# Optimization experiments

Measured on AMD Instinct MI355X. Metric: run time of the kernel, lower is better.

## Reference

```python
import jax, jax.numpy as jnp
import numpy as np

NODE_DIM = 128
OUT_DIM = 64
N_NODES = 50000
N_EDGES = 800000
NEG_SLOPE = 0.01  # F.leaky_relu default


def setup_inputs() -> dict:
    key = jax.random.key(0)
    k1, k2, k3, k4, k5 = jax.random.split(key, 5)
    h = jax.random.normal(k1, (N_NODES, NODE_DIM), dtype=jnp.float32)
    src = jax.random.randint(k2, (N_EDGES,), 0, N_NODES, dtype=jnp.int32)
    dst = jax.random.randint(k3, (N_EDGES,), 0, N_NODES, dtype=jnp.int32)
    # fc: Linear(node_dim, out_dim, bias=False); attn_fc: Linear(2*out_dim, 1, bias=False)
    W_fc = jax.random.normal(k4, (NODE_DIM, OUT_DIM), dtype=jnp.float32) * (1.0 / np.sqrt(NODE_DIM))
    W_attn = jax.random.normal(k5, (2 * OUT_DIM, 1), dtype=jnp.float32) * (1.0 / np.sqrt(2 * OUT_DIM))
    return {"h": h, "src": src, "dst": dst, "W_fc": W_fc, "W_attn": W_attn}


def reference(h, src, dst, W_fc, W_attn):
    N = h.shape[0]
    D = W_fc.shape[1]
    z = h @ W_fc                                   # [N, D]
    # attn_fc(concat(z_src, z_dst)) == z_src @ Wa[:D] + z_dst @ Wa[D:]
    s_src = (z @ W_attn[:D]).squeeze(-1)            # [N]
    s_dst = (z @ W_attn[D:]).squeeze(-1)            # [N]
    e = jax.nn.leaky_relu(s_src[src] + s_dst[dst], NEG_SLOPE)  # [E]
    # segment softmax over incoming edges per dst node
    m = jax.ops.segment_max(e, dst, num_segments=N)            # [N]
    ex = jnp.exp(e - m[dst])                                   # [E]
    denom = jax.ops.segment_sum(ex, dst, num_segments=N)       # [N]
    alpha = ex / denom[dst]                                    # [E]
    # weighted scatter-sum of src features into dst nodes
    out = jax.ops.segment_sum(alpha[:, None] * z[src], dst, num_segments=N)  # [N, D]
    return out
```

## Files before the change

kernel.cpp:

```cpp
#include <hip/hip_runtime.h>

#define NODE_DIM 128
#define OUT_DIM  64
#define NEG_SLOPE 0.01f
#define EPB   4096
#define BSH   7
#define NPB   128
#define CAPC  40
#define MAXB  2400

typedef __attribute__((ext_vector_type(8))) short short8;
typedef __attribute__((ext_vector_type(4))) short short4v;
typedef __attribute__((ext_vector_type(4))) float float4e;

__device__ __forceinline__ unsigned short f2bf(float f) {
    unsigned u = __float_as_uint(f);
    unsigned r = (u + 0x7FFFu + ((u >> 16) & 1u)) >> 16;
    return (unsigned short)r;
}
__device__ __forceinline__ float bf2f(unsigned short v) {
    return __uint_as_float((unsigned)v << 16);
}
__device__ __forceinline__ void split_bf(float v, short& hi, short& lo) {
    unsigned short h = f2bf(v);
    float r = v - bf2f(h);
    hi = (short)h;
    lo = (short)f2bf(r);
}

__global__ __launch_bounds__(256) void k_proj_part(
    const float* __restrict__ h, const float* __restrict__ Wf,
    const float* __restrict__ Wa,
    unsigned short* __restrict__ zbf,
    float* __restrict__ s_src, float* __restrict__ s_dst,
    const int* __restrict__ src, const int* __restrict__ dst,
    int* __restrict__ chunks, int* __restrict__ bhist,
    int N, int E, int PB, int nblkP, int NB)
{
    __shared__ union {
        short w[16384];
        unsigned short zt[4][16][68];
    } uni;
    __shared__ int cnt[392];

    if (blockIdx.x >= (unsigned)PB) {
        const int blk = blockIdx.x - PB;
        const int t = threadIdx.x;
        for (int i = t; i < NB; i += 256) cnt[i] = 0;
        __syncthreads();
        const int e0 = blk * EPB + t * 16;
        if (e0 < E) {
            int ne = E - e0; if (ne > 16) ne = 16;
            if (ne == 16) {
                int db[16], sb[16];
                const int4* dp = (const int4*)(dst + e0);
                const int4* sp = (const int4*)(src + e0);
                #pragma unroll
                for (int q = 0; q < 4; ++q) {
                    int4 dv = dp[q], svv = sp[q];
                    db[q*4+0]=dv.x; db[q*4+1]=dv.y; db[q*4+2]=dv.z; db[q*4+3]=dv.w;
                    sb[q*4+0]=svv.x; sb[q*4+1]=svv.y; sb[q*4+2]=svv.z; sb[q*4+3]=svv.w;
                }
                #pragma unroll
                for (int k = 0; k < 16; ++k) {
                    int d = db[k];
                    int bk = d >> BSH;
                    int r = atomicAdd(&cnt[bk], 1);
                    if (r < CAPC)
                        chunks[((size_t)bk * nblkP + blk) * CAPC + r] = ((d & (NPB-1)) << 17) | sb[k];
                }
            } else {
                for (int k = 0; k < ne; ++k) {
                    int d = dst[e0 + k];
                    int bk = d >> BSH;
                    int r = atomicAdd(&cnt[bk], 1);
                    if (r < CAPC)
                        chunks[((size_t)bk * nblkP + blk) * CAPC + r] = ((d & (NPB-1)) << 17) | src[e0 + k];
                }
            }
        }
        __syncthreads();
        for (int i = t; i < NB; i += 256)
            bhist[i * nblkP + blk] = (cnt[i] < CAPC) ? cnt[i] : CAPC;
        return;
    }

    const int t    = threadIdx.x;
    const int wv   = t >> 6;
    const int lane = t & 63;
    const int m    = lane & 15;
    const int quad = lane >> 4;
    const int row0 = blockIdx.x * 64 + wv * 16;

    int rowc = row0 + m; if (rowc > N - 1) rowc = N - 1;
    const float* hrow = h + (size_t)rowc * NODE_DIM;
    float4e hreg[8];
    #pragma unroll
    for (int t4 = 0; t4 < 4; ++t4) {
        hreg[t4 * 2]     = *(const float4e*)(hrow + t4 * 32 + quad * 8);
        hreg[t4 * 2 + 1] = *(const float4e*)(hrow + t4 * 32 + quad * 8 + 4);
    }

    {
        short* wh = uni.w;
        short* wl = uni.w + 8192;
        for (int s = t; s < 1024; s += 256) {
            int combo = s >> 6;
            int ln    = s & 63;
            int c = combo >> 2, t4 = combo & 3;
            int col = c * 16 + (ln & 15);
            int kq  = t4 * 32 + (ln >> 4) * 8;
            #pragma unroll
            for (int j = 0; j < 8; ++j) {
                short hi, lo;
                split_bf(Wf[(kq + j) * OUT_DIM + col], hi, lo);
                wh[s * 8 + j] = hi;
                wl[s * 8 + j] = lo;
            }
        }
    }
    __syncthreads();

    short8 Ahi[4], Alo[4];
    #pragma unroll
    for (int t4 = 0; t4 < 4; ++t4) {
        #pragma unroll
        for (int j = 0; j < 4; ++j) {
            short hi, lo;
            split_bf(hreg[t4 * 2][j], hi, lo);
            Ahi[t4][j] = hi; Alo[t4][j] = lo;
            split_bf(hreg[t4 * 2 + 1][j], hi, lo);
            Ahi[t4][4 + j] = hi; Alo[t4][4 + j] = lo;
        }
    }

    float ps[4] = {0.f, 0.f, 0.f, 0.f};
    float pd[4] = {0.f, 0.f, 0.f, 0.f};
    unsigned short z16[16];

    const short* wh = uni.w;
    const short* wl = uni.w + 8192;
    #pragma unroll
    for (int c = 0; c < 4; ++c) {
        float4e acc = {0.f, 0.f, 0.f, 0.f};
        #pragma unroll
        for (int t4 = 0; t4 < 4; ++t4) {
            int slot = (c * 4 + t4) * 64 + lane;
            short8 bh = *(const short8*)(wh + slot * 8);
            short8 bl = *(const short8*)(wl + slot * 8);
            acc = __builtin_amdgcn_mfma_f32_16x16x32_bf16(Alo[t4], bh, acc, 0, 0, 0);
            acc = __builtin_amdgcn_mfma_f32_16x16x32_bf16(Ahi[t4], bl, acc, 0, 0, 0);
            acc = __builtin_amdgcn_mfma_f32_16x16x32_bf16(Ahi[t4], bh, acc, 0, 0, 0);
        }
        int col = c * 16 + m;
        float was = Wa[col];
        float wad = Wa[OUT_DIM + col];
        #pragma unroll
        for (int r = 0; r < 4; ++r) {
            z16[c * 4 + r] = f2bf(acc[r]);
            ps[r] = fmaf(acc[r], was, ps[r]);
            pd[r] = fmaf(acc[r], wad, pd[r]);
        }
    }

    #pragma unroll
    for (int r = 0; r < 4; ++r) {
        #pragma unroll
        for (int off = 1; off < 16; off <<= 1) {
            ps[r] += __shfl_xor(ps[r], off, 64);
            pd[r] += __shfl_xor(pd[r], off, 64);
        }
    }
    if (m == 0) {
        #pragma unroll
        for (int r = 0; r < 4; ++r) {
            int nrow = row0 + quad * 4 + r;
            if (nrow < N) { s_src[nrow] = ps[r]; s_dst[nrow] = pd[r]; }
        }
    }

    __syncthreads();
    {
        unsigned short (*zt)[68] = uni.zt[wv];
        #pragma unroll
        for (int c = 0; c < 4; ++c)
            #pragma unroll
            for (int r = 0; r < 4; ++r)
                zt[quad * 4 + r][c * 16 + m] = z16[c * 4 + r];
        short* zb = (short*)zbf;
        #pragma unroll
        for (int i = 0; i < 2; ++i) {
            int r    = i * 8 + (lane >> 3);
            int colb = (lane & 7) * 8;
            short8 zz = *(const short8*)&zt[r][colb];
            int grow = row0 + r;
            if (grow < N)
                *(short8*)(zb + (size_t)grow * OUT_DIM + colb) = zz;
        }
    }
}

__global__ __launch_bounds__(512) void k_bucket_agg(
    const int* __restrict__ chunks, const int* __restrict__ bhist,
    const float* __restrict__ s_src, const float* __restrict__ s_dst,
    const unsigned short* __restrict__ zbf,
    float* __restrict__ out, int N, int nblkP)
{
    __shared__ int   sSrc[MAXB];
    __shared__ float xs[MAXB];
    __shared__ int cntN[NPB], rsN[NPB], curN[NPB], sscan[NPB];
    const int b = blockIdx.x;
    const int t = threadIdx.x;
    const int wid = t >> 6, lane = t & 63;
    const int nodeBase = b * NPB;

    if (t < NPB) cntN[t] = 0;
    __syncthreads();

    for (int c = wid; c < nblkP; c += 8) {
        int cc = bhist[b * nblkP + c];
        if (lane < cc) {
            int val = chunks[((size_t)b * nblkP + c) * CAPC + lane];
            atomicAdd(&cntN[val >> 17], 1);
        }
    }
    __syncthreads();

    int vc = 0;
    if (t < NPB) { vc = cntN[t]; sscan[t] = vc; }
    __syncthreads();
    #pragma unroll
    for (int off = 1; off < NPB; off <<= 1) {
        int u = 0;
        if (t < NPB && t >= off) u = sscan[t - off];
        __syncthreads();
        if (t < NPB) sscan[t] += u;
        __syncthreads();
    }
    if (t < NPB) { rsN[t] = sscan[t] - vc; curN[t] = sscan[t] - vc; }
    __syncthreads();

    for (int c = wid; c < nblkP; c += 8) {
        int cc = bhist[b * nblkP + c];
        if (lane < cc) {
            int val = chunks[((size_t)b * nblkP + c) * CAPC + lane];
            int n7 = val >> 17;
            int sidx = val & 0x1FFFF;
            int pos = atomicAdd(&curN[n7], 1);
            if (pos < MAXB) {
                sSrc[pos] = sidx;
                float e = s_src[sidx] + s_dst[nodeBase + n7];
                e = (e > 0.f) ? e : e * NEG_SLOPE;
                xs[pos] = __expf(e);
            }
        }
    }
    __syncthreads();

    const short* zb = (const short*)zbf;
    const int cl8 = (lane & 15) * 4;
    #pragma unroll
    for (int pass = 0; pass < 4; ++pass) {
        int n7 = pass * 32 + wid * 4 + (lane >> 4);
        int node = nodeBase + n7;
        int rs = rsN[n7], dg = cntN[n7];
        if (rs + dg > MAXB) dg = (rs < MAXB) ? (MAXB - rs) : 0;
        float a0 = 0.f, a1 = 0.f, a2 = 0.f, a3 = 0.f, den = 0.f;
        int e = 0;
        for (; e + 4 <= dg; e += 4) {
            int i0 = rs + e;
            int ss0 = sSrc[i0], ss1 = sSrc[i0+1], ss2 = sSrc[i0+2], ss3 = sSrc[i0+3];
            float x0 = xs[i0], x1 = xs[i0+1], x2 = xs[i0+2], x3 = xs[i0+3];
            short4v z0 = *(const short4v*)(zb + ((size_t)(unsigned)ss0 << 6) + cl8);
            short4v z1 = *(const short4v*)(zb + ((size_t)(unsigned)ss1 << 6) + cl8);
            short4v z2 = *(const short4v*)(zb + ((size_t)(unsigned)ss2 << 6) + cl8);
            short4v z3 = *(const short4v*)(zb + ((size_t)(unsigned)ss3 << 6) + cl8);
            den += (x0 + x1) + (x2 + x3);
            a0 = fmaf(x0, bf2f((unsigned short)z0[0]), a0);
            a1 = fmaf(x0, bf2f((unsigned short)z0[1]), a1);
            a2 = fmaf(x0, bf2f((unsigned short)z0[2]), a2);
            a3 = fmaf(x0, bf2f((unsigned short)z0[3]), a3);
            a0 = fmaf(x1, bf2f((unsigned short)z1[0]), a0);
            a1 = fmaf(x1, bf2f((unsigned short)z1[1]), a1);
            a2 = fmaf(x1, bf2f((unsigned short)z1[2]), a2);
            a3 = fmaf(x1, bf2f((unsigned short)z1[3]), a3);
            a0 = fmaf(x2, bf2f((unsigned short)z2[0]), a0);
            a1 = fmaf(x2, bf2f((unsigned short)z2[1]), a1);
            a2 = fmaf(x2, bf2f((unsigned short)z2[2]), a2);
            a3 = fmaf(x2, bf2f((unsigned short)z2[3]), a3);
            a0 = fmaf(x3, bf2f((unsigned short)z3[0]), a0);
            a1 = fmaf(x3, bf2f((unsigned short)z3[1]), a1);
            a2 = fmaf(x3, bf2f((unsigned short)z3[2]), a2);
            a3 = fmaf(x3, bf2f((unsigned short)z3[3]), a3);
        }
        for (; e < dg; ++e) {
            int i0 = rs + e;
            int ss0 = sSrc[i0];
            float x0 = xs[i0];
            short4v z0 = *(const short4v*)(zb + ((size_t)(unsigned)ss0 << 6) + cl8);
            den += x0;
            a0 = fmaf(x0, bf2f((unsigned short)z0[0]), a0);
            a1 = fmaf(x0, bf2f((unsigned short)z0[1]), a1);
            a2 = fmaf(x0, bf2f((unsigned short)z0[2]), a2);
            a3 = fmaf(x0, bf2f((unsigned short)z0[3]), a3);
        }
        if (node < N) {
            float4e o;
            if (dg > 0) {
                float inv = 1.f / den;
                o[0] = a0 * inv; o[1] = a1 * inv; o[2] = a2 * inv; o[3] = a3 * inv;
            } else {
                o[0] = 0.f; o[1] = 0.f; o[2] = 0.f; o[3] = 0.f;
            }
            *(float4e*)(out + (size_t)node * OUT_DIM + cl8) = o;
        }
    }
}

extern "C" void kernel_launch(void* const* d_in, const int* in_sizes, int n_in,
                              void* d_out, int out_size, void* d_ws, size_t ws_size,
                              hipStream_t stream) {
    const float* h   = (const float*)d_in[0];
    const int*   src = (const int*)d_in[1];
    const int*   dst = (const int*)d_in[2];
    const float* Wf  = (const float*)d_in[3];
    const float* Wa  = (const float*)d_in[4];
    const int N = in_sizes[0] / NODE_DIM;
    const int E = in_sizes[1];
    float* out = (float*)d_out;

    const int PB    = (N + 63) / 64;
    const int nblkP = (E + EPB - 1) / EPB;
    const int NB    = (N + NPB - 1) / NPB;

    char* ws = (char*)d_ws;
    size_t off = 0;
    int* chunks = (int*)(ws + off);             off += (size_t)NB * nblkP * CAPC * sizeof(int);
    int* bhist  = (int*)(ws + off);             off += (size_t)NB * nblkP * sizeof(int);
    unsigned short* zbf = (unsigned short*)(ws + off); off += (size_t)N * OUT_DIM * sizeof(unsigned short);
    float* s_src = (float*)(ws + off);          off += (size_t)N * sizeof(float);
    float* s_dst = (float*)(ws + off);          off += (size_t)N * sizeof(float);

    k_proj_part<<<PB + nblkP, 256, 0, stream>>>(h, Wf, Wa, zbf, s_src, s_dst,
                                                src, dst, chunks, bhist, N, E, PB, nblkP, NB);
    k_bucket_agg<<<NB, 512, 0, stream>>>(chunks, bhist, s_src, s_dst, zbf, out, N, nblkP);
}
```

Measured before the change: 136.3 us.

## Replace fixed-capacity per-block chunks with compacted per-bucket regions via global atomics

The partition blocks now sort their edges by bucket in shared memory with a local prefix scan. Each block then reserves a contiguous range in a per-bucket global region through atomicAdd on a bucket cursor and writes its edges there coalesced. The aggregation kernel reads one dense region per bucket instead of scanning many sparsely filled fixed-capacity chunks, which removes padded reads and the per-chunk histogram walk. The cost is a memset, global atomics, and a heavier partition phase that is now scheduled first in the grid. Edge order within a bucket becomes nondeterministic, so the float summation order can vary between runs.

```diff
diff --git a/kernel.cpp b/kernel.cpp
--- a/kernel.cpp
+++ b/kernel.cpp
@@ -3,11 +3,10 @@
 #define NODE_DIM 128
 #define OUT_DIM  64
 #define NEG_SLOPE 0.01f
-#define EPB   4096
-#define BSH   7
-#define NPB   128
-#define CAPC  40
-#define MAXB  2400
+#define EPB    4096
+#define BSH    7
+#define NPB    128
+#define REGCAP 2400
 
 typedef __attribute__((ext_vector_type(8))) short short8;
 typedef __attribute__((ext_vector_type(4))) short short4v;
@@ -34,63 +33,101 @@
     unsigned short* __restrict__ zbf,
     float* __restrict__ s_src, float* __restrict__ s_dst,
     const int* __restrict__ src, const int* __restrict__ dst,
-    int* __restrict__ chunks, int* __restrict__ bhist,
-    int N, int E, int PB, int nblkP, int NB)
+    int* __restrict__ region, int* __restrict__ bcur,
+    int N, int E, int nblkP, int NB)
 {
     __shared__ union {
         short w[16384];
         unsigned short zt[4][16][68];
+        struct { int sd[EPB]; int sv[EPB]; } p;
     } uni;
-    __shared__ int cnt[392];
-
-    if (blockIdx.x >= (unsigned)PB) {
-        const int blk = blockIdx.x - PB;
+    __shared__ int cnt[512];
+    __shared__ int bb[512];
+    __shared__ int rr[512];
+    __shared__ int ps[256];
+
+    if (blockIdx.x < (unsigned)nblkP) {
+        const int blk = blockIdx.x;
         const int t = threadIdx.x;
-        for (int i = t; i < NB; i += 256) cnt[i] = 0;
-        __syncthreads();
-        const int e0 = blk * EPB + t * 16;
-        if (e0 < E) {
-            int ne = E - e0; if (ne > 16) ne = 16;
-            if (ne == 16) {
-                int db[16], sb[16];
-                const int4* dp = (const int4*)(dst + e0);
-                const int4* sp = (const int4*)(src + e0);
-                #pragma unroll
-                for (int q = 0; q < 4; ++q) {
-                    int4 dv = dp[q], svv = sp[q];
-                    db[q*4+0]=dv.x; db[q*4+1]=dv.y; db[q*4+2]=dv.z; db[q*4+3]=dv.w;
-                    sb[q*4+0]=svv.x; sb[q*4+1]=svv.y; sb[q*4+2]=svv.z; sb[q*4+3]=svv.w;
+        cnt[t] = 0; cnt[t + 256] = 0;
+        __syncthreads();
+        const int e0 = blk * EPB;
+        int nE = E - e0; if (nE > EPB) nE = EPB;
+
+        int db[16], sb[16], rreg[16];
+        const int base = e0 + t * 16;
+        if (base + 16 <= E) {
+            const int4* dp = (const int4*)(dst + base);
+            const int4* sp = (const int4*)(src + base);
+            #pragma unroll
+            for (int q = 0; q < 4; ++q) {
+                int4 dv = dp[q], svv = sp[q];
+                db[q*4+0]=dv.x; db[q*4+1]=dv.y; db[q*4+2]=dv.z; db[q*4+3]=dv.w;
+                sb[q*4+0]=svv.x; sb[q*4+1]=svv.y; sb[q*4+2]=svv.z; sb[q*4+3]=svv.w;
+            }
+            #pragma unroll
+            for (int k = 0; k < 16; ++k)
+                rreg[k] = atomicAdd(&cnt[db[k] >> BSH], 1);
+        } else {
+            #pragma unroll
+            for (int k = 0; k < 16; ++k) rreg[k] = -1;
+            for (int k = 0; k < 16; ++k) {
+                int idx = base + k;
+                if (idx < E) {
+                    db[k] = dst[idx];
+                    sb[k] = src[idx];
+                    rreg[k] = atomicAdd(&cnt[db[k] >> BSH], 1);
                 }
-                #pragma unroll
-                for (int k = 0; k < 16; ++k) {
-                    int d = db[k];
-                    int bk = d >> BSH;
-                    int r = atomicAdd(&cnt[bk], 1);
-                    if (r < CAPC)
-                        chunks[((size_t)bk * nblkP + blk) * CAPC + r] = ((d & (NPB-1)) << 17) | sb[k];
-                }
-            } else {
-                for (int k = 0; k < ne; ++k) {
-                    int d = dst[e0 + k];
-                    int bk = d >> BSH;
-                    int r = atomicAdd(&cnt[bk], 1);
-                    if (r < CAPC)
-                        chunks[((size_t)bk * nblkP + blk) * CAPC + r] = ((d & (NPB-1)) << 17) | src[e0 + k];
-                }
-            }
-        }
-        __syncthreads();
-        for (int i = t; i < NB; i += 256)
-            bhist[i * nblkP + blk] = (cnt[i] < CAPC) ? cnt[i] : CAPC;
+            }
+        }
+        __syncthreads();
+
+        int pv = cnt[2 * t] + cnt[2 * t + 1];
+        ps[t] = pv;
+        __syncthreads();
+        #pragma unroll
+        for (int off = 1; off < 256; off <<= 1) {
+            int u = (t >= off) ? ps[t - off] : 0;
+            __syncthreads();
+            ps[t] += u;
+            __syncthreads();
+        }
+        int pexc = ps[t] - pv;
+        bb[2 * t]     = pexc;
+        bb[2 * t + 1] = pexc + cnt[2 * t];
+        __syncthreads();
+
+        #pragma unroll
+        for (int k = 0; k < 16; ++k) {
+            if (rreg[k] >= 0) {
+                int pos = bb[db[k] >> BSH] + rreg[k];
+                uni.p.sd[pos] = db[k];
+                uni.p.sv[pos] = sb[k];
+            }
+        }
+        for (int i = t; i < NB; i += 256) {
+            int cb = cnt[i];
+            rr[i] = cb ? atomicAdd(bcur + i, cb) : 0;
+        }
+        __syncthreads();
+
+        for (int j = t; j < nE; j += 256) {
+            int d = uni.p.sd[j];
+            int b = d >> BSH;
+            int gp = rr[b] + (j - bb[b]);
+            if (gp < REGCAP)
+                region[(size_t)b * REGCAP + gp] = ((d & (NPB - 1)) << 17) | uni.p.sv[j];
+        }
         return;
     }
 
+    const int bid  = blockIdx.x - nblkP;
     const int t    = threadIdx.x;
     const int wv   = t >> 6;
     const int lane = t & 63;
     const int m    = lane & 15;
     const int quad = lane >> 4;
-    const int row0 = blockIdx.x * 64 + wv * 16;
+    const int row0 = bid * 64 + wv * 16;
 
     int rowc = row0 + m; if (rowc > N - 1) rowc = N - 1;
     const float* hrow = h + (size_t)rowc * NODE_DIM;
@@ -134,8 +171,8 @@
         }
     }
 
-    float ps[4] = {0.f, 0.f, 0.f, 0.f};
-    float pd[4] = {0.f, 0.f, 0.f, 0.f};
+    float psum[4] = {0.f, 0.f, 0.f, 0.f};
+    float pdum[4] = {0.f, 0.f, 0.f, 0.f};
     unsigned short z16[16];
 
     const short* wh = uni.w;
@@ -158,8 +195,8 @@
         #pragma unroll
         for (int r = 0; r < 4; ++r) {
             z16[c * 4 + r] = f2bf(acc[r]);
-            ps[r] = fmaf(acc[r], was, ps[r]);
-            pd[r] = fmaf(acc[r], wad, pd[r]);
+            psum[r] = fmaf(acc[r], was, psum[r]);
+            pdum[r] = fmaf(acc[r], wad, pdum[r]);
         }
     }
 
@@ -167,15 +204,15 @@
     for (int r = 0; r < 4; ++r) {
         #pragma unroll
         for (int off = 1; off < 16; off <<= 1) {
-            ps[r] += __shfl_xor(ps[r], off, 64);
-            pd[r] += __shfl_xor(pd[r], off, 64);
+            psum[r] += __shfl_xor(psum[r], off, 64);
+            pdum[r] += __shfl_xor(pdum[r], off, 64);
         }
     }
     if (m == 0) {
         #pragma unroll
         for (int r = 0; r < 4; ++r) {
             int nrow = row0 + quad * 4 + r;
-            if (nrow < N) { s_src[nrow] = ps[r]; s_dst[nrow] = pd[r]; }
+            if (nrow < N) { s_src[nrow] = psum[r]; s_dst[nrow] = pdum[r]; }
         }
     }
 
@@ -201,29 +238,26 @@
 }
 
 __global__ __launch_bounds__(512) void k_bucket_agg(
-    const int* __restrict__ chunks, const int* __restrict__ bhist,
+    const int* __restrict__ region, const int* __restrict__ bcur,
     const float* __restrict__ s_src, const float* __restrict__ s_dst,
     const unsigned short* __restrict__ zbf,
-    float* __restrict__ out, int N, int nblkP)
+    float* __restrict__ out, int N)
 {
-    __shared__ int   sSrc[MAXB];
-    __shared__ float xs[MAXB];
+    __shared__ int   sSrc[REGCAP];
+    __shared__ float xs[REGCAP];
     __shared__ int cntN[NPB], rsN[NPB], curN[NPB], sscan[NPB];
     const int b = blockIdx.x;
     const int t = threadIdx.x;
-    const int wid = t >> 6, lane = t & 63;
     const int nodeBase = b * NPB;
 
+    int total = bcur[b];
+    if (total > REGCAP) total = REGCAP;
     if (t < NPB) cntN[t] = 0;
     __syncthreads();
 
-    for (int c = wid; c < nblkP; c += 8) {
-        int cc = bhist[b * nblkP + c];
-        if (lane < cc) {
-            int val = chunks[((size_t)b * nblkP + c) * CAPC + lane];
-            atomicAdd(&cntN[val >> 17], 1);
-        }
-    }
+    const int* reg = region + (size_t)b * REGCAP;
+    for (int i = t; i < total; i += 512)
+        atomicAdd(&cntN[reg[i] >> 17], 1);
     __syncthreads();
 
     int vc = 0;
@@ -240,31 +274,26 @@
     if (t < NPB) { rsN[t] = sscan[t] - vc; curN[t] = sscan[t] - vc; }
     __syncthreads();
 
-    for (int c = wid; c < nblkP; c += 8) {
-        int cc = bhist[b * nblkP + c];
-        if (lane < cc) {
-            int val = chunks[((size_t)b * nblkP + c) * CAPC + lane];
-            int n7 = val >> 17;
-            int sidx = val & 0x1FFFF;
-            int pos = atomicAdd(&curN[n7], 1);
-            if (pos < MAXB) {
-                sSrc[pos] = sidx;
-                float e = s_src[sidx] + s_dst[nodeBase + n7];
-                e = (e > 0.f) ? e : e * NEG_SLOPE;
-                xs[pos] = __expf(e);
-            }
-        }
+    for (int i = t; i < total; i += 512) {
+        int val = reg[i];
+        int n7 = val >> 17;
+        int sidx = val & 0x1FFFF;
+        int pos = atomicAdd(&curN[n7], 1);
+        sSrc[pos] = sidx;
+        float e = s_src[sidx] + s_dst[nodeBase + n7];
+        e = (e > 0.f) ? e : e * NEG_SLOPE;
+        xs[pos] = __expf(e);
     }
     __syncthreads();
 
     const short* zb = (const short*)zbf;
+    const int lane = t & 63, wid = t >> 6;
     const int cl8 = (lane & 15) * 4;
     #pragma unroll
     for (int pass = 0; pass < 4; ++pass) {
         int n7 = pass * 32 + wid * 4 + (lane >> 4);
         int node = nodeBase + n7;
         int rs = rsN[n7], dg = cntN[n7];
-        if (rs + dg > MAXB) dg = (rs < MAXB) ? (MAXB - rs) : 0;
         float a0 = 0.f, a1 = 0.f, a2 = 0.f, a3 = 0.f, den = 0.f;
         int e = 0;
         for (; e + 4 <= dg; e += 4) {
@@ -335,13 +364,14 @@
 
     char* ws = (char*)d_ws;
     size_t off = 0;
-    int* chunks = (int*)(ws + off);             off += (size_t)NB * nblkP * CAPC * sizeof(int);
-    int* bhist  = (int*)(ws + off);             off += (size_t)NB * nblkP * sizeof(int);
+    int* region = (int*)(ws + off);             off += (size_t)NB * REGCAP * sizeof(int);
+    int* bcur   = (int*)(ws + off);             off += (size_t)NB * sizeof(int);
     unsigned short* zbf = (unsigned short*)(ws + off); off += (size_t)N * OUT_DIM * sizeof(unsigned short);
     float* s_src = (float*)(ws + off);          off += (size_t)N * sizeof(float);
     float* s_dst = (float*)(ws + off);          off += (size_t)N * sizeof(float);
 
-    k_proj_part<<<PB + nblkP, 256, 0, stream>>>(h, Wf, Wa, zbf, s_src, s_dst,
-                                                src, dst, chunks, bhist, N, E, PB, nblkP, NB);
-    k_bucket_agg<<<NB, 512, 0, stream>>>(chunks, bhist, s_src, s_dst, zbf, out, N, nblkP);
-}
+    hipMemsetAsync(bcur, 0, (size_t)NB * sizeof(int), stream);
+    k_proj_part<<<nblkP + PB, 256, 0, stream>>>(h, Wf, Wa, zbf, s_src, s_dst,
+                                                src, dst, region, bcur, N, E, nblkP, NB);
+    k_bucket_agg<<<NB, 512, 0, stream>>>(region, bcur, s_src, s_dst, zbf, out, N);
+}
```

Result: faster. 122.2 us (-10.3%).
